# Kernel tuning notes

Measured on AMD Instinct MI355X. Metric: run time of the kernel, lower is better.

Reference implementation:

```python
import math
import jax, jax.numpy as jnp
import numpy as np

N_HEADS = 16
HIDDEN = 1024
FACTOR = 256
N_DK = HIDDEN // N_HEADS
B, S = 4, 2048


def _linear_params(key, fan_in, fan_out):
    kw, kb = jax.random.split(key)
    bound = 1.0 / math.sqrt(fan_in)
    W = jax.random.uniform(kw, (fan_in, fan_out), jnp.float32, -bound, bound)
    b = jax.random.uniform(kb, (fan_out,), jnp.float32, -bound, bound)
    return W, b


def setup_inputs() -> dict:
    key = jax.random.key(0)
    ks = jax.random.split(key, 12)
    inp = {
        "query": jax.random.normal(ks[0], (B, S, HIDDEN), jnp.float32),
        "key": jax.random.normal(ks[1], (B, S, HIDDEN), jnp.float32),
        "value": jax.random.normal(ks[2], (B, S, HIDDEN), jnp.float32),
        "mask": jax.random.randint(ks[3], (B, S), 0, 2, jnp.int32),
    }
    names = [("pq", HIDDEN, FACTOR), ("tq", FACTOR, HIDDEN),
             ("pk", HIDDEN, FACTOR), ("tk", FACTOR, HIDDEN),
             ("pv", HIDDEN, FACTOR), ("tv", FACTOR, HIDDEN),
             ("po", HIDDEN, FACTOR), ("to", FACTOR, HIDDEN)]
    for i, (nm, fi, fo) in enumerate(names):
        W, b = _linear_params(ks[4 + i], fi, fo)
        inp[f"W{nm}"], inp[f"b{nm}"] = W, b
    return inp


def _factored(x, Wp, bp, Wt, bt):
    # proj -> leaky_relu(0.2) -> tran
    h = jax.nn.leaky_relu(x @ Wp + bp, negative_slope=0.2)
    return h @ Wt + bt


def reference(query, key, value, mask,
              Wpq, bpq, Wtq, btq, Wpk, bpk, Wtk, btk,
              Wpv, bpv, Wtv, btv, Wpo, bpo, Wto, bto):
    bsize = query.shape[0]

    def split_heads(x):  # [B,S,H*Dk] -> [B,H,S,Dk]
        return x.reshape(bsize, -1, N_HEADS, N_DK).transpose(0, 2, 1, 3)

    q = split_heads(_factored(query, Wpq, bpq, Wtq, btq))
    k = split_heads(_factored(key, Wpk, bpk, Wtk, btk))
    v = split_heads(_factored(value, Wpv, bpv, Wtv, btv))

    scores = jnp.einsum("bhqd,bhkd->bhqk", q, k) / math.sqrt(N_DK)
    m = (mask == 0)[:, None, None, :]  # [B,1,1,S]
    scores = jnp.where(m, jnp.float32(-1e20), scores)
    attn = jax.nn.softmax(scores, axis=-1)
    cv = jnp.einsum("bhqk,bhkd->bhqd", attn, v)
    cv = cv.transpose(0, 2, 1, 3).reshape(bsize, -1, N_HEADS * N_DK)
    # dropout omitted (eval mode / deterministic reference)
    return _factored(cv, Wpo, bpo, Wto, bto)
```

## Files before the change

### kernel.cpp

```cpp
#include <hip/hip_runtime.h>
#include <cstdint>
#include <cstddef>

typedef __bf16 bf16_t;
typedef __bf16 bf16x8 __attribute__((ext_vector_type(8)));
typedef float  f32x4  __attribute__((ext_vector_type(4)));
typedef unsigned int uint32x4 __attribute__((ext_vector_type(4)));
typedef unsigned int uint32x2 __attribute__((ext_vector_type(2)));

#define DEV_INLINE __device__ __forceinline__

constexpr int Bsz = 4, Ssz = 2048, HID = 1024, FAC = 256, NH = 16, DKc = 64;
constexpr int Mrows = Bsz * Ssz;
constexpr float QSCALE = 0.18033688011112042f;

struct Ptr8 { const float* p[8]; };
struct Ptr3 { const float* p[3]; };

DEV_INLINE float fast_exp2(float x) {
#if __has_builtin(__builtin_amdgcn_exp2f)
  return __builtin_amdgcn_exp2f(x);
#else
  return exp2f(x);
#endif
}

DEV_INLINE void async16(const void* g, void* l) {
  __builtin_amdgcn_global_load_lds((const __attribute__((address_space(1))) void*)g,
                                   (__attribute__((address_space(3))) void*)l, 16, 0, 0);
}

#define WBAR(N) do { \
  asm volatile("s_waitcnt vmcnt(" #N ") lgkmcnt(0)" ::: "memory"); \
  __builtin_amdgcn_s_barrier(); \
} while (0)

DEV_INLINE int SW(int r) { return (r & 3) | ((r >> 1) & 4); }

__global__ __launch_bounds__(256) void k_prep(Ptr8 w, Ptr8 bsrc, const int* __restrict__ mask,
                                              bf16_t* wpt, bf16_t* wtt,
                                              float* bp, float* bt, float* mf, bf16_t* mb) {
  const int z = blockIdx.z;
  if (z == 8) {
    const int bid = blockIdx.y * 32 + blockIdx.x;
    if (bid >= 64) return;
    const int i = bid * 256 + threadIdx.x;
    if (i < 4 * FAC) bp[i] = bsrc.p[i >> 8][i & 255];
    if (i < 4 * HID) bt[i] = bsrc.p[4 + (i >> 10)][i & 1023];
    if (i < Bsz * Ssz) {
      const float m = (mask[i] != 0) ? 1.f : 0.f;
      mf[i] = m;
      mb[i] = (bf16_t)m;
    }
    return;
  }
  const int K = (z < 4) ? HID : FAC;
  const int N = (z < 4) ? FAC : HID;
  if ((int)(blockIdx.x * 32) >= N || (int)(blockIdx.y * 32) >= K) return;
  __shared__ float t[32][33];
  const float* src = w.p[z];
  bf16_t* dst = (z < 4) ? (wpt + (size_t)z * FAC * HID) : (wtt + (size_t)(z - 4) * FAC * HID);
  const int tx = threadIdx.x & 31, ty = threadIdx.x >> 5;
  const int kb = blockIdx.y * 32, nb = blockIdx.x * 32;
#pragma unroll
  for (int j = 0; j < 4; ++j)
    t[ty + j * 8][tx] = src[(size_t)(kb + ty + j * 8) * N + nb + tx];
  __syncthreads();
#pragma unroll
  for (int j = 0; j < 4; ++j)
    dst[(size_t)(nb + ty + j * 8) * K + kb + tx] = (bf16_t)t[tx][ty + j * 8];
}

__global__ __launch_bounds__(256, 2) void k_gemmP2(Ptr3 Asrc,
                                                   const bf16_t* __restrict__ Bt_,
                                                   const float* __restrict__ biasAll,
                                                   bf16_t* __restrict__ Call) {
  __shared__ __align__(16) bf16_t As[3][64 * 40];
  __shared__ __align__(16) bf16_t Bs[4][128 * 32];

  const int z = blockIdx.z;
  const bf16_t* Bt = Bt_ + (size_t)z * FAC * HID;
  const float* bias = biasAll + z * FAC;
  bf16_t* C = Call + (size_t)z * Mrows * FAC;

  const int tid = threadIdx.x;
  const int lane = tid & 63, wave = tid >> 6;
  const int quad = lane >> 4, l16 = lane & 15;
  const int m0 = blockIdx.y * 64, n0 = blockIdx.x * 128;

  const int brow = wave * 16 + (lane >> 2), bkc = (lane & 3) * 8;
  const bf16_t* gB0 = Bt + (size_t)(n0 + brow) * HID + bkc;
  const bf16_t* gB1 = gB0 + (size_t)64 * HID;

  const int crow = tid >> 2, chalf = (tid & 3) * 8;
  const float* gAf = Asrc.p[z] + (size_t)(m0 + crow) * HID + chalf;

#define ASYNCB(t, buf)                                \
  do {                                                \
    const int k0_ = (t) * 32;                         \
    async16(gB0 + k0_, Bs[buf] + wave * 512);         \
    async16(gB1 + k0_, Bs[buf] + 2048 + wave * 512);  \
  } while (0)

  {
    f32x4 pa = *(const f32x4*)gAf;
    f32x4 pb = *(const f32x4*)(gAf + 4);
    __builtin_amdgcn_sched_barrier(0);
    ASYNCB(0, 0);
    ASYNCB(1, 1);
    union { bf16_t h[8]; uint32x4 u; } o;
#pragma unroll
    for (int j = 0; j < 4; ++j) { o.h[j] = (bf16_t)pa[j]; o.h[4 + j] = (bf16_t)pb[j]; }
    *(uint32x4*)(As[0] + crow * 40 + chalf) = o.u;
  }

  f32x4 acc[4][2] = {};
  constexpr int nk = 32;

  for (int it = 0; it < nk; ++it) {
    f32x4 xa, xb;
    const int k1 = (it + 1) * 32;
    if (it + 1 < nk) {
      xa = *(const f32x4*)(gAf + k1);
      xb = *(const f32x4*)(gAf + k1 + 4);
    }
    __builtin_amdgcn_sched_barrier(0);
    if (it + 2 < nk) ASYNCB(it + 2, (it + 2) & 3);

    if (it + 2 < nk)      WBAR(6);
    else if (it + 1 < nk) WBAR(4);
    else                  WBAR(0);

    const bf16_t* Ac = As[it % 3];
    const bf16_t* Bc = Bs[it & 3];
    bf16x8 af[4], bfr[2];
#pragma unroll
    for (int i = 0; i < 4; ++i)
      af[i] = *(const bf16x8*)(Ac + (i * 16 + l16) * 40 + quad * 8);
#pragma unroll
    for (int i = 0; i < 2; ++i)
      bfr[i] = *(const bf16x8*)(Bc + (wave * 32 + i * 16 + l16) * 32 + quad * 8);
#pragma unroll
    for (int mi = 0; mi < 4; ++mi)
#pragma unroll
      for (int ni = 0; ni < 2; ++ni)
        acc[mi][ni] = __builtin_amdgcn_mfma_f32_16x16x32_bf16(af[mi], bfr[ni], acc[mi][ni], 0, 0, 0);

    if (it + 1 < nk) {
      union { bf16_t h[8]; uint32x4 u; } o;
#pragma unroll
      for (int j = 0; j < 4; ++j) { o.h[j] = (bf16_t)xa[j]; o.h[4 + j] = (bf16_t)xb[j]; }
      *(uint32x4*)(As[(it + 1) % 3] + crow * 40 + chalf) = o.u;
    }
  }
#undef ASYNCB

#pragma unroll
  for (int mi = 0; mi < 4; ++mi) {
    const int rbase = m0 + mi * 16 + quad * 4;
#pragma unroll
    for (int ni = 0; ni < 2; ++ni) {
      const int col = n0 + wave * 32 + ni * 16 + l16;
      const float bv = bias[col];
#pragma unroll
      for (int r = 0; r < 4; ++r) {
        float y = acc[mi][ni][r] + bv;
        y = (y > 0.f) ? y : 0.2f * y;
        C[(size_t)(rbase + r) * FAC + col] = (bf16_t)y;
      }
    }
  }
}

template <int EPI, typename OUT_T>
__global__ __launch_bounds__(256, 2) void k_gemmQ(const bf16_t* __restrict__ Aall,
                                                  const bf16_t* __restrict__ Btall,
                                                  const float* __restrict__ biasAll,
                                                  OUT_T* __restrict__ Call,
                                                  bf16_t* __restrict__ C2,
                                                  const float* __restrict__ rowmul,
                                                  int N, int K,
                                                  long long Az, long long Bz, long long Cz, int biasz) {
  __shared__ __align__(16) bf16_t As[4][128 * 32];
  __shared__ __align__(16) bf16_t Bs[4][128 * 32];

  const int z = blockIdx.z;
  const bf16_t* Bt = Btall + (size_t)z * Bz;
  const float* bias = biasAll + (size_t)z * biasz;
  OUT_T* C = Call + (size_t)z * Cz;

  const int tid = threadIdx.x;
  const int lane = tid & 63, wave = tid >> 6;
  const int quad = lane >> 4, l16 = lane & 15;
  const int wr = wave >> 1, wc = wave & 1;
  const int m0 = blockIdx.y * 128, n0 = blockIdx.x * 128;

  const int arow = wave * 16 + (lane >> 2), akc = (lane & 3) * 8;
  const bf16_t* gB0 = Bt + (size_t)(n0 + arow) * K + akc;
  const bf16_t* gB1 = gB0 + (size_t)64 * K;
  const bf16_t* A = Aall + (size_t)z * Az;
  const bf16_t* gA0 = A + (size_t)(m0 + arow) * K + akc;
  const bf16_t* gA1 = gA0 + (size_t)64 * K;

#define STAGEQ(t, buf)                               \
  do {                                               \
    const int k0_ = (t) * 32;                        \
    async16(gA0 + k0_, As[buf] + wave * 512);        \
    async16(gA1 + k0_, As[buf] + 2048 + wave * 512); \
    async16(gB0 + k0_, Bs[buf] + wave * 512);        \
    async16(gB1 + k0_, Bs[buf] + 2048 + wave * 512); \
  } while (0)

  const int nk = K / 32;
  STAGEQ(0, 0);
  STAGEQ(1, 1);

  f32x4 acc[4][4] = {};

  for (int it = 0; it < nk; ++it) {
    if (it + 2 < nk) STAGEQ(it + 2, (it + 2) & 3);

    if (it + 2 < nk)      WBAR(8);
    else if (it + 1 < nk) WBAR(4);
    else                  WBAR(0);

    const bf16_t* Ac = As[it & 3];
    const bf16_t* Bc = Bs[it & 3];
    bf16x8 af[4], bfr[4];
#pragma unroll
    for (int i = 0; i < 4; ++i)
      af[i] = *(const bf16x8*)(Ac + (wr * 64 + i * 16 + l16) * 32 + quad * 8);
#pragma unroll
    for (int i = 0; i < 4; ++i)
      bfr[i] = *(const bf16x8*)(Bc + (wc * 64 + i * 16 + l16) * 32 + quad * 8);
#pragma unroll
    for (int mi = 0; mi < 4; ++mi)
#pragma unroll
      for (int ni = 0; ni < 4; ++ni)
        acc[mi][ni] = __builtin_amdgcn_mfma_f32_16x16x32_bf16(af[mi], bfr[ni], acc[mi][ni], 0, 0, 0);
  }
#undef STAGEQ

  if (EPI == 1 && z == 2) {
#pragma unroll
    for (int mi = 0; mi < 4; ++mi) {
      const int rbase = m0 + wr * 64 + mi * 16 + quad * 4;
      const int bb = rbase >> 11, s = rbase & 2047;
      float rmv[4];
#pragma unroll
      for (int r = 0; r < 4; ++r) rmv[r] = rowmul[rbase + r];
#pragma unroll
      for (int ni = 0; ni < 4; ++ni) {
        const int col = n0 + wc * 64 + ni * 16 + l16;
        const float bv = bias[col];
        const int hh = col >> 6, d = col & 63;
        union { bf16_t e[4]; uint32x2 u; } p;
#pragma unroll
        for (int r = 0; r < 4; ++r) p.e[r] = (bf16_t)((acc[mi][ni][r] + bv) * rmv[r]);
        *(uint32x2*)(C2 + (((size_t)((bb * NH + hh) * DKc + d)) << 11) + s) = p.u;
      }
    }
    return;
  }

  const float scale = (EPI == 1 && z == 0) ? QSCALE : 1.f;
#pragma unroll
  for (int mi = 0; mi < 4; ++mi) {
    const int rbase = m0 + wr * 64 + mi * 16 + quad * 4;
#pragma unroll
    for (int ni = 0; ni < 4; ++ni) {
      const int col = n0 + wc * 64 + ni * 16 + l16;
      const float bv = bias[col];
#pragma unroll
      for (int r = 0; r < 4; ++r) {
        float y = (acc[mi][ni][r] + bv) * scale;
        if (EPI == 0) y = (y > 0.f) ? y : 0.2f * y;
        C[(size_t)(rbase + r) * N + col] = (OUT_T)y;
      }
    }
  }
}

__global__ __launch_bounds__(512, 2) void k_attn(const bf16_t* __restrict__ qkv,
                                                 const bf16_t* __restrict__ mb,
                                                 bf16_t* __restrict__ cv) {
  __shared__ __align__(16) bf16_t Ks[4][64 * 64];
  __shared__ __align__(16) bf16_t Vt[4][64 * 64];
  __shared__ __align__(16) bf16_t Ml[Ssz];

  const int qt = blockIdx.x, h = blockIdx.y, b = blockIdx.z;
  const bf16_t* qp = qkv;
  const bf16_t* kp = qkv + (size_t)Mrows * HID;
  const bf16_t* vtp = qkv + 2 * (size_t)Mrows * HID + (size_t)(b * NH + h) * DKc * Ssz;

  const int tid = threadIdx.x;
  const int lane = tid & 63, wave = tid >> 6;
  const int quad = lane >> 4, l16 = lane & 15;

  const int r0 = wave * 8 + (lane >> 3);
  const int c0 = ((lane & 7) ^ SW(r0)) * 8;
  const int ldsOff = wave * 512;
  const bf16_t* kgA = kp + (size_t)(b * Ssz + r0) * HID + h * DKc + c0;
  const bf16_t* vgA = vtp + (size_t)r0 * Ssz + c0;

#define STAGEA(t, buf)                                          \
  do {                                                          \
    async16(kgA + (size_t)(t) * 64 * HID, Ks[buf] + ldsOff);    \
    async16(vgA + (t) * 64, Vt[buf] + ldsOff);                  \
  } while (0)

  *(uint32x2*)(Ml + tid * 4) = *(const uint32x2*)(mb + (size_t)b * Ssz + tid * 4);
  STAGEA(0, 0);
  STAGEA(1, 1);

  bf16x8 aq0[4], aq1[4];
#pragma unroll
  for (int g = 0; g < 4; ++g) {
    const size_t qrow = (size_t)(b * Ssz + qt * 512 + g * 128 + wave * 16 + l16) * HID + h * DKc + quad * 8;
    aq0[g] = *(const bf16x8*)(qp + qrow);
    aq1[g] = *(const bf16x8*)(qp + qrow + 32);
  }

  const int krow = 8 * (l16 >> 2) + (l16 & 3);
  f32x4 acc[4][4] = {};
  f32x4 dacc[4] = {};
  const bf16x8 zfrag = {};

  for (int kt = 0; kt < 32; ++kt) {
    if (kt + 2 < 32) STAGEA(kt + 2, (kt + 2) & 3);

    if (kt + 2 < 32)      WBAR(4);
    else if (kt + 1 < 32) WBAR(2);
    else                  WBAR(0);

    const bf16_t* Kc = Ks[kt & 3];
    const bf16_t* Vc = Vt[kt & 3];

    union U { uint32x4 u; bf16x8 h; } ap0[4], ap1[4];
    constexpr int koff[4] = {0, 4, 32, 36};
#pragma unroll
    for (int ks = 0; ks < 4; ++ks) {
      const int row = krow + koff[ks];
      const int sw = SW(row);
      bf16x8 a0 = *(const bf16x8*)(Kc + row * 64 + (quad ^ sw) * 8);
      bf16x8 a1 = *(const bf16x8*)(Kc + row * 64 + ((quad + 4) ^ sw) * 8);
#pragma unroll
      for (int g = 0; g < 4; ++g) {
        f32x4 c = {};
        c = __builtin_amdgcn_mfma_f32_16x16x32_bf16(a0, aq0[g], c, 0, 0, 0);
        c = __builtin_amdgcn_mfma_f32_16x16x32_bf16(a1, aq1[g], c, 0, 0, 0);
        union { bf16_t h[2]; uint32_t u; } p01, p23;
        p01.h[0] = (bf16_t)fast_exp2(c[0]);
        p01.h[1] = (bf16_t)fast_exp2(c[1]);
        p23.h[0] = (bf16_t)fast_exp2(c[2]);
        p23.h[1] = (bf16_t)fast_exp2(c[3]);
        U& t = (ks < 2) ? ap0[g] : ap1[g];
        t.u[(ks & 1) * 2] = p01.u;
        t.u[(ks & 1) * 2 + 1] = p23.u;
      }
    }

    bf16x8 mr0 = *(const bf16x8*)(Ml + kt * 64 + quad * 8);
    bf16x8 mr1 = *(const bf16x8*)(Ml + kt * 64 + 32 + quad * 8);
    if (l16 != 0) { mr0 = zfrag; mr1 = zfrag; }
#pragma unroll
    for (int g = 0; g < 4; ++g) {
      dacc[g] = __builtin_amdgcn_mfma_f32_16x16x32_bf16(ap0[g].h, mr0, dacc[g], 0, 0, 0);
      dacc[g] = __builtin_amdgcn_mfma_f32_16x16x32_bf16(ap1[g].h, mr1, dacc[g], 0, 0, 0);
    }

#pragma unroll
    for (int d = 0; d < 4; ++d) {
      const int row = d * 16 + l16;
      const int sw = SW(row);
      bf16x8 bv0 = *(const bf16x8*)(Vc + row * 64 + (quad ^ sw) * 8);
      bf16x8 bv1 = *(const bf16x8*)(Vc + row * 64 + ((quad + 4) ^ sw) * 8);
#pragma unroll
      for (int g = 0; g < 4; ++g) {
        acc[g][d] = __builtin_amdgcn_mfma_f32_16x16x32_bf16(ap0[g].h, bv0, acc[g][d], 0, 0, 0);
        acc[g][d] = __builtin_amdgcn_mfma_f32_16x16x32_bf16(ap1[g].h, bv1, acc[g][d], 0, 0, 0);
      }
    }
  }
#undef STAGEA

#pragma unroll
  for (int g = 0; g < 4; ++g) {
    const size_t obase = (size_t)(b * Ssz + qt * 512 + g * 128 + wave * 16 + quad * 4) * HID + h * DKc + l16;
#pragma unroll
    for (int r = 0; r < 4; ++r) {
      const float denom = __shfl(dacc[g][r], lane & 48, 64);
      const float rl = 1.f / denom;
#pragma unroll
      for (int d = 0; d < 4; ++d)
        cv[obase + (size_t)r * HID + d * 16] = (bf16_t)(acc[g][d][r] * rl);
    }
  }
}

extern "C" void kernel_launch(void* const* d_in, const int* in_sizes, int n_in,
                              void* d_out, int out_size, void* d_ws, size_t ws_size,
                              hipStream_t stream) {
  (void)in_sizes; (void)n_in; (void)out_size; (void)ws_size;
  const float* q_in = (const float*)d_in[0];
  const float* k_in = (const float*)d_in[1];
  const float* v_in = (const float*)d_in[2];
  const int* mask = (const int*)d_in[3];

  bf16_t* XB = (bf16_t*)d_ws;
  bf16_t* H3 = XB + (size_t)3 * Mrows * HID;
  bf16_t* CV = H3 + (size_t)3 * Mrows * FAC;
  bf16_t* WPT = CV + (size_t)Mrows * HID;
  bf16_t* WTT = WPT + (size_t)4 * FAC * HID;
  float* BP = (float*)(WTT + (size_t)4 * FAC * HID);
  float* BT = BP + 4 * FAC;
  float* MF = BT + 4 * HID;
  bf16_t* MB = (bf16_t*)(MF + Mrows);
  bf16_t* VTg = XB + 2 * (size_t)Mrows * HID;

  Ptr8 w;
  w.p[0] = (const float*)d_in[4];  w.p[1] = (const float*)d_in[8];
  w.p[2] = (const float*)d_in[12]; w.p[3] = (const float*)d_in[16];
  w.p[4] = (const float*)d_in[6];  w.p[5] = (const float*)d_in[10];
  w.p[6] = (const float*)d_in[14]; w.p[7] = (const float*)d_in[18];
  Ptr8 bs;
  bs.p[0] = (const float*)d_in[5];  bs.p[1] = (const float*)d_in[9];
  bs.p[2] = (const float*)d_in[13]; bs.p[3] = (const float*)d_in[17];
  bs.p[4] = (const float*)d_in[7];  bs.p[5] = (const float*)d_in[11];
  bs.p[6] = (const float*)d_in[15]; bs.p[7] = (const float*)d_in[19];
  hipLaunchKernelGGL(k_prep, dim3(32, 32, 9), dim3(256), 0, stream, w, bs, mask,
                     WPT, WTT, BP, BT, MF, MB);

  Ptr3 xs; xs.p[0] = q_in; xs.p[1] = k_in; xs.p[2] = v_in;

  hipLaunchKernelGGL(k_gemmP2, dim3(2, Mrows / 64, 3), dim3(256), 0, stream,
                     xs, WPT, BP, H3);

  hipLaunchKernelGGL((k_gemmQ<1, bf16_t>), dim3(HID / 128, Mrows / 128, 3), dim3(256), 0, stream,
                     H3, WTT, BT, XB, VTg, MF,
                     HID, FAC, (long long)Mrows * FAC, (long long)FAC * HID, (long long)Mrows * HID, HID);

  hipLaunchKernelGGL(k_attn, dim3(Ssz / 512, NH, Bsz), dim3(512), 0, stream, XB, MB, CV);

  hipLaunchKernelGGL((k_gemmQ<0, bf16_t>), dim3(FAC / 128, Mrows / 128, 1), dim3(256), 0, stream,
                     CV, WPT + (size_t)3 * FAC * HID, BP + 3 * FAC, H3, (bf16_t*)nullptr,
                     (const float*)nullptr, FAC, HID, 0LL, 0LL, 0LL, 0);

  hipLaunchKernelGGL((k_gemmQ<2, float>), dim3(HID / 128, Mrows / 128, 1), dim3(256), 0, stream,
                     H3, WTT + (size_t)3 * FAC * HID, BT + 3 * HID, (float*)d_out, (bf16_t*)nullptr,
                     (const float*)nullptr, HID, FAC, 0LL, 0LL, 0LL, 0);
}
```

Before: 339.0 us.

## Fuse factored proj and tran GEMMs into one kernel with LDS-resident hidden

Replaces the separate projection and transform GEMM kernels with a single fused kernel, used both for the Q/K/V projections and for the output projection. Each block computes a 128-row slab of the leaky-ReLU hidden activations, keeps it in shared memory, and then streams the transform weights through a pipelined loop to produce the full output width. The intent is to remove the global-memory round trip for the hidden tensor and two kernel launches, and an XOR swizzle is added to the LDS tile layout to reduce bank conflicts. In exchange the grid shrinks to 192 blocks for Q/K/V and 64 for the output path, and the large shared-memory footprint likely limits residency to one block per CU, which risks leaving many CUs idle.

```diff
diff --git a/kernel.cpp b/kernel.cpp
--- a/kernel.cpp
+++ b/kernel.cpp
@@ -36,15 +36,15 @@
 } while (0)
 
 DEV_INLINE int SW(int r) { return (r & 3) | ((r >> 1) & 4); }
+DEV_INLINE int SW32(int r) { return (r >> 1) & 3; }
 
 __global__ __launch_bounds__(256) void k_prep(Ptr8 w, Ptr8 bsrc, const int* __restrict__ mask,
                                               bf16_t* wpt, bf16_t* wtt,
                                               float* bp, float* bt, float* mf, bf16_t* mb) {
   const int z = blockIdx.z;
   if (z == 8) {
-    const int bid = blockIdx.y * 32 + blockIdx.x;
-    if (bid >= 64) return;
-    const int i = bid * 256 + threadIdx.x;
+    if (blockIdx.x >= 64) return;
+    const int i = blockIdx.x * 256 + threadIdx.x;
     if (i < 4 * FAC) bp[i] = bsrc.p[i >> 8][i & 255];
     if (i < 4 * HID) bt[i] = bsrc.p[4 + (i >> 10)][i & 1023];
     if (i < Bsz * Ssz) {
@@ -56,12 +56,12 @@
   }
   const int K = (z < 4) ? HID : FAC;
   const int N = (z < 4) ? FAC : HID;
-  if ((int)(blockIdx.x * 32) >= N || (int)(blockIdx.y * 32) >= K) return;
+  const int nbN = N / 32;
+  const int nb = (blockIdx.x % nbN) * 32, kb = (blockIdx.x / nbN) * 32;
   __shared__ float t[32][33];
   const float* src = w.p[z];
   bf16_t* dst = (z < 4) ? (wpt + (size_t)z * FAC * HID) : (wtt + (size_t)(z - 4) * FAC * HID);
   const int tx = threadIdx.x & 31, ty = threadIdx.x >> 5;
-  const int kb = blockIdx.y * 32, nb = blockIdx.x * 32;
 #pragma unroll
   for (int j = 0; j < 4; ++j)
     t[ty + j * 8][tx] = src[(size_t)(kb + ty + j * 8) * N + nb + tx];
@@ -71,214 +71,231 @@
     dst[(size_t)(nb + ty + j * 8) * K + kb + tx] = (bf16_t)t[tx][ty + j * 8];
 }
 
-__global__ __launch_bounds__(256, 2) void k_gemmP2(Ptr3 Asrc,
-                                                   const bf16_t* __restrict__ Bt_,
-                                                   const float* __restrict__ biasAll,
-                                                   bf16_t* __restrict__ Call) {
-  __shared__ __align__(16) bf16_t As[3][64 * 40];
-  __shared__ __align__(16) bf16_t Bs[4][128 * 32];
-
-  const int z = blockIdx.z;
-  const bf16_t* Bt = Bt_ + (size_t)z * FAC * HID;
-  const float* bias = biasAll + z * FAC;
-  bf16_t* C = Call + (size_t)z * Mrows * FAC;
+template <int CAST_A, int QKV, typename OUT_T>
+__global__ __launch_bounds__(512, 2) void k_fact2(Ptr3 Asrc, const bf16_t* __restrict__ Abf,
+                                                  const bf16_t* __restrict__ WpB,
+                                                  const float* __restrict__ bpB,
+                                                  const bf16_t* __restrict__ WtB,
+                                                  const float* __restrict__ btB,
+                                                  OUT_T* __restrict__ CoutAll,
+                                                  bf16_t* __restrict__ C2,
+                                                  const float* __restrict__ rowmul) {
+  constexpr int LDTA = CAST_A ? 40 : 32;
+  __shared__ __align__(16) bf16_t smem[128 * 264 + 4 * 256 * 32];
+  bf16_t* As = smem;
+  bf16_t* Hl = smem;
+  bf16_t* Bs = smem + 128 * 264;
+
+  const int z = QKV ? blockIdx.z : 0;
+  const bf16_t* Wp = WpB + (size_t)z * FAC * HID;
+  const float* bp = bpB + z * FAC;
+  const bf16_t* Wt = WtB + (size_t)z * FAC * HID;
+  const float* bt = btB + z * HID;
+  OUT_T* Cout = QKV ? (CoutAll + (size_t)z * Mrows * HID) : CoutAll;
 
   const int tid = threadIdx.x;
   const int lane = tid & 63, wave = tid >> 6;
   const int quad = lane >> 4, l16 = lane & 15;
-  const int m0 = blockIdx.y * 64, n0 = blockIdx.x * 128;
-
-  const int brow = wave * 16 + (lane >> 2), bkc = (lane & 3) * 8;
-  const bf16_t* gB0 = Bt + (size_t)(n0 + brow) * HID + bkc;
-  const bf16_t* gB1 = gB0 + (size_t)64 * HID;
+  const int swl = SW32(l16);
+  const int m0 = blockIdx.x * 128;
+
+  const int b1row = wave * 32 + (lane >> 2);
+  const int bslot = (((lane & 3) ^ SW32(b1row)) & 3) * 8;
+  const int wOff = wave * 1024;
+  const bf16_t* gW0 = Wp + (size_t)b1row * HID + bslot;
+  const bf16_t* gW1 = gW0 + (size_t)16 * HID;
 
   const int crow = tid >> 2, chalf = (tid & 3) * 8;
-  const float* gAf = Asrc.p[z] + (size_t)(m0 + crow) * HID + chalf;
-
-#define ASYNCB(t, buf)                                \
-  do {                                                \
-    const int k0_ = (t) * 32;                         \
-    async16(gB0 + k0_, Bs[buf] + wave * 512);         \
-    async16(gB1 + k0_, Bs[buf] + 2048 + wave * 512);  \
+  const float* gAf = nullptr;
+  const bf16_t* gAb = nullptr;
+  if (CAST_A) {
+    gAf = Asrc.p[z] + (size_t)(m0 + crow) * HID + chalf;
+  } else {
+    const int arowA = wave * 16 + (lane >> 2);
+    const int aslot = (((lane & 3) ^ SW32(arowA)) & 3) * 8;
+    gAb = Abf + (size_t)(m0 + arowA) * HID + aslot;
+  }
+
+#define STB1(t)                                              \
+  do {                                                       \
+    const int k0_ = (t) * 32;                                \
+    bf16_t* d_ = Bs + ((t) & 3) * 8192 + wOff;               \
+    async16(gW0 + k0_, d_);                                  \
+    async16(gW1 + k0_, d_ + 512);                            \
   } while (0)
-
-  {
+#define STA1(t) async16(gAb + (t) * 32, As + ((t) & 3) * 4096 + wave * 512)
+
+  if (CAST_A) {
     f32x4 pa = *(const f32x4*)gAf;
     f32x4 pb = *(const f32x4*)(gAf + 4);
     __builtin_amdgcn_sched_barrier(0);
-    ASYNCB(0, 0);
-    ASYNCB(1, 1);
+    STB1(0);
+    STB1(1);
     union { bf16_t h[8]; uint32x4 u; } o;
 #pragma unroll
     for (int j = 0; j < 4; ++j) { o.h[j] = (bf16_t)pa[j]; o.h[4 + j] = (bf16_t)pb[j]; }
-    *(uint32x4*)(As[0] + crow * 40 + chalf) = o.u;
-  }
-
-  f32x4 acc[4][2] = {};
+    *(uint32x4*)(As + crow * LDTA + chalf) = o.u;
+  } else {
+    STA1(0); STB1(0);
+    STA1(1); STB1(1);
+  }
+
+  f32x4 acc[8][2] = {};
   constexpr int nk = 32;
 
   for (int it = 0; it < nk; ++it) {
-    f32x4 xa, xb;
-    const int k1 = (it + 1) * 32;
-    if (it + 1 < nk) {
-      xa = *(const f32x4*)(gAf + k1);
-      xb = *(const f32x4*)(gAf + k1 + 4);
-    }
-    __builtin_amdgcn_sched_barrier(0);
-    if (it + 2 < nk) ASYNCB(it + 2, (it + 2) & 3);
-
-    if (it + 2 < nk)      WBAR(6);
-    else if (it + 1 < nk) WBAR(4);
-    else                  WBAR(0);
-
-    const bf16_t* Ac = As[it % 3];
-    const bf16_t* Bc = Bs[it & 3];
-    bf16x8 af[4], bfr[2];
-#pragma unroll
-    for (int i = 0; i < 4; ++i)
-      af[i] = *(const bf16x8*)(Ac + (i * 16 + l16) * 40 + quad * 8);
-#pragma unroll
-    for (int i = 0; i < 2; ++i)
-      bfr[i] = *(const bf16x8*)(Bc + (wave * 32 + i * 16 + l16) * 32 + quad * 8);
-#pragma unroll
-    for (int mi = 0; mi < 4; ++mi)
-#pragma unroll
-      for (int ni = 0; ni < 2; ++ni)
-        acc[mi][ni] = __builtin_amdgcn_mfma_f32_16x16x32_bf16(af[mi], bfr[ni], acc[mi][ni], 0, 0, 0);
-
-    if (it + 1 < nk) {
-      union { bf16_t h[8]; uint32x4 u; } o;
-#pragma unroll
-      for (int j = 0; j < 4; ++j) { o.h[j] = (bf16_t)xa[j]; o.h[4 + j] = (bf16_t)xb[j]; }
-      *(uint32x4*)(As[(it + 1) % 3] + crow * 40 + chalf) = o.u;
-    }
-  }
-#undef ASYNCB
-
-#pragma unroll
-  for (int mi = 0; mi < 4; ++mi) {
-    const int rbase = m0 + mi * 16 + quad * 4;
+    if (CAST_A) {
+      f32x4 xa, xb;
+      const int k1 = (it + 1) * 32;
+      if (it + 1 < nk) {
+        xa = *(const f32x4*)(gAf + k1);
+        xb = *(const f32x4*)(gAf + k1 + 4);
+      }
+      __builtin_amdgcn_sched_barrier(0);
+      if (it + 2 < nk) STB1(it + 2);
+      if (it + 2 < nk)      WBAR(6);
+      else if (it + 1 < nk) WBAR(4);
+      else                  WBAR(0);
+
+      const bf16_t* Ac = As + (it % 3) * (128 * 40);
+      const bf16_t* Bc = Bs + (it & 3) * 8192;
+      bf16x8 af[8], bfr[2];
+#pragma unroll
+      for (int i = 0; i < 8; ++i)
+        af[i] = *(const bf16x8*)(Ac + (i * 16 + l16) * LDTA + quad * 8);
+#pragma unroll
+      for (int i = 0; i < 2; ++i)
+        bfr[i] = *(const bf16x8*)(Bc + (wave * 32 + i * 16 + l16) * 32 + ((quad ^ swl) & 3) * 8);
+#pragma unroll
+      for (int mi = 0; mi < 8; ++mi)
+#pragma unroll
+        for (int ni = 0; ni < 2; ++ni)
+          acc[mi][ni] = __builtin_amdgcn_mfma_f32_16x16x32_bf16(af[mi], bfr[ni], acc[mi][ni], 0, 0, 0);
+
+      if (it + 1 < nk) {
+        union { bf16_t h[8]; uint32x4 u; } o;
+#pragma unroll
+        for (int j = 0; j < 4; ++j) { o.h[j] = (bf16_t)xa[j]; o.h[4 + j] = (bf16_t)xb[j]; }
+        *(uint32x4*)(As + ((it + 1) % 3) * (128 * 40) + crow * LDTA + chalf) = o.u;
+      }
+    } else {
+      if (it + 2 < nk) { STA1(it + 2); STB1(it + 2); }
+      if (it + 2 < nk)      WBAR(6);
+      else if (it + 1 < nk) WBAR(3);
+      else                  WBAR(0);
+
+      const bf16_t* Ac = As + (it & 3) * 4096;
+      const bf16_t* Bc = Bs + (it & 3) * 8192;
+      bf16x8 af[8], bfr[2];
+#pragma unroll
+      for (int i = 0; i < 8; ++i)
+        af[i] = *(const bf16x8*)(Ac + (i * 16 + l16) * LDTA + ((quad ^ swl) & 3) * 8);
+#pragma unroll
+      for (int i = 0; i < 2; ++i)
+        bfr[i] = *(const bf16x8*)(Bc + (wave * 32 + i * 16 + l16) * 32 + ((quad ^ swl) & 3) * 8);
+#pragma unroll
+      for (int mi = 0; mi < 8; ++mi)
+#pragma unroll
+        for (int ni = 0; ni < 2; ++ni)
+          acc[mi][ni] = __builtin_amdgcn_mfma_f32_16x16x32_bf16(af[mi], bfr[ni], acc[mi][ni], 0, 0, 0);
+    }
+  }
+#undef STA1
+
+  __syncthreads();
+#pragma unroll
+  for (int mi = 0; mi < 8; ++mi)
 #pragma unroll
     for (int ni = 0; ni < 2; ++ni) {
-      const int col = n0 + wave * 32 + ni * 16 + l16;
-      const float bv = bias[col];
+      const int col = wave * 32 + ni * 16 + l16;
+      const float bv = bp[col];
 #pragma unroll
       for (int r = 0; r < 4; ++r) {
         float y = acc[mi][ni][r] + bv;
         y = (y > 0.f) ? y : 0.2f * y;
-        C[(size_t)(rbase + r) * FAC + col] = (bf16_t)y;
-      }
-    }
-  }
-}
-
-template <int EPI, typename OUT_T>
-__global__ __launch_bounds__(256, 2) void k_gemmQ(const bf16_t* __restrict__ Aall,
-                                                  const bf16_t* __restrict__ Btall,
-                                                  const float* __restrict__ biasAll,
-                                                  OUT_T* __restrict__ Call,
-                                                  bf16_t* __restrict__ C2,
-                                                  const float* __restrict__ rowmul,
-                                                  int N, int K,
-                                                  long long Az, long long Bz, long long Cz, int biasz) {
-  __shared__ __align__(16) bf16_t As[4][128 * 32];
-  __shared__ __align__(16) bf16_t Bs[4][128 * 32];
-
-  const int z = blockIdx.z;
-  const bf16_t* Bt = Btall + (size_t)z * Bz;
-  const float* bias = biasAll + (size_t)z * biasz;
-  OUT_T* C = Call + (size_t)z * Cz;
-
-  const int tid = threadIdx.x;
-  const int lane = tid & 63, wave = tid >> 6;
-  const int quad = lane >> 4, l16 = lane & 15;
-  const int wr = wave >> 1, wc = wave & 1;
-  const int m0 = blockIdx.y * 128, n0 = blockIdx.x * 128;
-
-  const int arow = wave * 16 + (lane >> 2), akc = (lane & 3) * 8;
-  const bf16_t* gB0 = Bt + (size_t)(n0 + arow) * K + akc;
-  const bf16_t* gB1 = gB0 + (size_t)64 * K;
-  const bf16_t* A = Aall + (size_t)z * Az;
-  const bf16_t* gA0 = A + (size_t)(m0 + arow) * K + akc;
-  const bf16_t* gA1 = gA0 + (size_t)64 * K;
-
-#define STAGEQ(t, buf)                               \
-  do {                                               \
-    const int k0_ = (t) * 32;                        \
-    async16(gA0 + k0_, As[buf] + wave * 512);        \
-    async16(gA1 + k0_, As[buf] + 2048 + wave * 512); \
-    async16(gB0 + k0_, Bs[buf] + wave * 512);        \
-    async16(gB1 + k0_, Bs[buf] + 2048 + wave * 512); \
+        Hl[(mi * 16 + quad * 4 + r) * 264 + col] = (bf16_t)y;
+      }
+      acc[mi][ni] = (f32x4){0.f, 0.f, 0.f, 0.f};
+    }
+  __syncthreads();
+
+#define STG2(ci)                                                              \
+  do {                                                                        \
+    const int nb_ = ((ci) >> 3) * 256, k0_ = ((ci) & 7) * 32;                 \
+    const bf16_t* g_ = Wt + (size_t)(nb_ + b1row) * FAC + k0_ + bslot;        \
+    bf16_t* d_ = Bs + ((ci) & 3) * 8192 + wOff;                               \
+    async16(g_, d_);                                                          \
+    async16(g_ + 16 * FAC, d_ + 512);                                         \
   } while (0)
 
-  const int nk = K / 32;
-  STAGEQ(0, 0);
-  STAGEQ(1, 1);
-
-  f32x4 acc[4][4] = {};
-
-  for (int it = 0; it < nk; ++it) {
-    if (it + 2 < nk) STAGEQ(it + 2, (it + 2) & 3);
-
-    if (it + 2 < nk)      WBAR(8);
-    else if (it + 1 < nk) WBAR(4);
+  STG2(0);
+  STG2(1);
+
+  for (int ci = 0; ci < 32; ++ci) {
+    if (ci + 2 < 32) STG2(ci + 2);
+    if (ci + 2 < 32)      WBAR(4);
+    else if (ci + 1 < 32) WBAR(2);
     else                  WBAR(0);
 
-    const bf16_t* Ac = As[it & 3];
-    const bf16_t* Bc = Bs[it & 3];
-    bf16x8 af[4], bfr[4];
-#pragma unroll
-    for (int i = 0; i < 4; ++i)
-      af[i] = *(const bf16x8*)(Ac + (wr * 64 + i * 16 + l16) * 32 + quad * 8);
-#pragma unroll
-    for (int i = 0; i < 4; ++i)
-      bfr[i] = *(const bf16x8*)(Bc + (wc * 64 + i * 16 + l16) * 32 + quad * 8);
-#pragma unroll
-    for (int mi = 0; mi < 4; ++mi)
-#pragma unroll
-      for (int ni = 0; ni < 4; ++ni)
+    const bf16_t* Bc = Bs + (ci & 3) * 8192;
+    const int k0 = (ci & 7) * 32;
+    bf16x8 af[8], bfr[2];
+#pragma unroll
+    for (int i = 0; i < 8; ++i)
+      af[i] = *(const bf16x8*)(Hl + (i * 16 + l16) * 264 + k0 + quad * 8);
+#pragma unroll
+    for (int i = 0; i < 2; ++i)
+      bfr[i] = *(const bf16x8*)(Bc + (wave * 32 + i * 16 + l16) * 32 + ((quad ^ swl) & 3) * 8);
+#pragma unroll
+    for (int mi = 0; mi < 8; ++mi)
+#pragma unroll
+      for (int ni = 0; ni < 2; ++ni)
         acc[mi][ni] = __builtin_amdgcn_mfma_f32_16x16x32_bf16(af[mi], bfr[ni], acc[mi][ni], 0, 0, 0);
-  }
-#undef STAGEQ
-
-  if (EPI == 1 && z == 2) {
-#pragma unroll
-    for (int mi = 0; mi < 4; ++mi) {
-      const int rbase = m0 + wr * 64 + mi * 16 + quad * 4;
-      const int bb = rbase >> 11, s = rbase & 2047;
-      float rmv[4];
-#pragma unroll
-      for (int r = 0; r < 4; ++r) rmv[r] = rowmul[rbase + r];
-#pragma unroll
-      for (int ni = 0; ni < 4; ++ni) {
-        const int col = n0 + wc * 64 + ni * 16 + l16;
-        const float bv = bias[col];
-        const int hh = col >> 6, d = col & 63;
-        union { bf16_t e[4]; uint32x2 u; } p;
-#pragma unroll
-        for (int r = 0; r < 4; ++r) p.e[r] = (bf16_t)((acc[mi][ni][r] + bv) * rmv[r]);
-        *(uint32x2*)(C2 + (((size_t)((bb * NH + hh) * DKc + d)) << 11) + s) = p.u;
-      }
-    }
-    return;
-  }
-
-  const float scale = (EPI == 1 && z == 0) ? QSCALE : 1.f;
-#pragma unroll
-  for (int mi = 0; mi < 4; ++mi) {
-    const int rbase = m0 + wr * 64 + mi * 16 + quad * 4;
-#pragma unroll
-    for (int ni = 0; ni < 4; ++ni) {
-      const int col = n0 + wc * 64 + ni * 16 + l16;
-      const float bv = bias[col];
-#pragma unroll
-      for (int r = 0; r < 4; ++r) {
-        float y = (acc[mi][ni][r] + bv) * scale;
-        if (EPI == 0) y = (y > 0.f) ? y : 0.2f * y;
-        C[(size_t)(rbase + r) * N + col] = (OUT_T)y;
-      }
-    }
-  }
+
+    if ((ci & 7) == 7) {
+      const int nbase = (ci >> 3) * 256;
+      if (QKV && z == 2) {
+#pragma unroll
+        for (int mi = 0; mi < 8; ++mi) {
+          const int rbase = m0 + mi * 16 + quad * 4;
+          const int bb = rbase >> 11, s = rbase & 2047;
+          float rmv[4];
+#pragma unroll
+          for (int r = 0; r < 4; ++r) rmv[r] = rowmul[rbase + r];
+#pragma unroll
+          for (int ni = 0; ni < 2; ++ni) {
+            const int col = nbase + wave * 32 + ni * 16 + l16;
+            const float bv = bt[col];
+            const int hh = col >> 6, d = col & 63;
+            union { bf16_t e[4]; uint32x2 u; } p;
+#pragma unroll
+            for (int r = 0; r < 4; ++r) p.e[r] = (bf16_t)((acc[mi][ni][r] + bv) * rmv[r]);
+            *(uint32x2*)(C2 + (((size_t)((bb * NH + hh) * DKc + d)) << 11) + s) = p.u;
+          }
+        }
+      } else {
+        const float scale = (QKV && z == 0) ? QSCALE : 1.f;
+#pragma unroll
+        for (int mi = 0; mi < 8; ++mi) {
+          const int row = m0 + mi * 16 + quad * 4;
+#pragma unroll
+          for (int ni = 0; ni < 2; ++ni) {
+            const int col = nbase + wave * 32 + ni * 16 + l16;
+            const float bv = bt[col];
+#pragma unroll
+            for (int r = 0; r < 4; ++r)
+              Cout[(size_t)(row + r) * HID + col] = (OUT_T)((acc[mi][ni][r] + bv) * scale);
+          }
+        }
+      }
+#pragma unroll
+      for (int mi = 0; mi < 8; ++mi)
+#pragma unroll
+        for (int ni = 0; ni < 2; ++ni) acc[mi][ni] = (f32x4){0.f, 0.f, 0.f, 0.f};
+    }
+  }
+#undef STG2
+#undef STB1
 }
 
 __global__ __launch_bounds__(512, 2) void k_attn(const bf16_t* __restrict__ qkv,
@@ -428,25 +445,19 @@
   bs.p[2] = (const float*)d_in[13]; bs.p[3] = (const float*)d_in[17];
   bs.p[4] = (const float*)d_in[7];  bs.p[5] = (const float*)d_in[11];
   bs.p[6] = (const float*)d_in[15]; bs.p[7] = (const float*)d_in[19];
-  hipLaunchKernelGGL(k_prep, dim3(32, 32, 9), dim3(256), 0, stream, w, bs, mask,
+  hipLaunchKernelGGL(k_prep, dim3(256, 1, 9), dim3(256), 0, stream, w, bs, mask,
                      WPT, WTT, BP, BT, MF, MB);
 
   Ptr3 xs; xs.p[0] = q_in; xs.p[1] = k_in; xs.p[2] = v_in;
-
-  hipLaunchKernelGGL(k_gemmP2, dim3(2, Mrows / 64, 3), dim3(256), 0, stream,
-                     xs, WPT, BP, H3);
-
-  hipLaunchKernelGGL((k_gemmQ<1, bf16_t>), dim3(HID / 128, Mrows / 128, 3), dim3(256), 0, stream,
-                     H3, WTT, BT, XB, VTg, MF,
-                     HID, FAC, (long long)Mrows * FAC, (long long)FAC * HID, (long long)Mrows * HID, HID);
+  Ptr3 nullp; nullp.p[0] = nullp.p[1] = nullp.p[2] = nullptr;
+
+  hipLaunchKernelGGL((k_fact2<1, 1, bf16_t>), dim3(Mrows / 128, 1, 3), dim3(512), 0, stream,
+                     xs, (const bf16_t*)nullptr, WPT, BP, WTT, BT, XB, VTg, MF);
 
   hipLaunchKernelGGL(k_attn, dim3(Ssz / 512, NH, Bsz), dim3(512), 0, stream, XB, MB, CV);
 
-  hipLaunchKernelGGL((k_gemmQ<0, bf16_t>), dim3(FAC / 128, Mrows / 128, 1), dim3(256), 0, stream,
-                     CV, WPT + (size_t)3 * FAC * HID, BP + 3 * FAC, H3, (bf16_t*)nullptr,
-                     (const float*)nullptr, FAC, HID, 0LL, 0LL, 0LL, 0);
-
-  hipLaunchKernelGGL((k_gemmQ<2, float>), dim3(HID / 128, Mrows / 128, 1), dim3(256), 0, stream,
-                     H3, WTT + (size_t)3 * FAC * HID, BT + 3 * HID, (float*)d_out, (bf16_t*)nullptr,
-                     (const float*)nullptr, HID, FAC, 0LL, 0LL, 0LL, 0);
-}
+  hipLaunchKernelGGL((k_fact2<0, 0, float>), dim3(Mrows / 128, 1, 1), dim3(512), 0, stream,
+                     nullp, CV, WPT + (size_t)3 * FAC * HID, BP + 3 * FAC,
+                     WTT + (size_t)3 * FAC * HID, BT + 3 * HID,
+                     (float*)d_out, (bf16_t*)nullptr, (const float*)nullptr);
+}
```

Result: no change. 332.8 us (-1.8%).
